# Optimization experiments

Measured on AMD Instinct MI355X. Metric: run time of the kernel, lower is better.

Reference implementation:

```python
import jax, jax.numpy as jnp
import numpy as np
from jax import lax

N_EXPERTS = 256
N_GROUP = 8
TOPK_GROUP = 4
TOP_K = 8
AUX_ALPHA = 0.001


def setup_inputs() -> dict:
    key = jax.random.key(0)
    k1, k2 = jax.random.split(key)
    hidden_states = jax.random.normal(k1, (16384, 2048), dtype=jnp.float32)
    weight = jax.random.normal(k2, (N_EXPERTS, 2048), dtype=jnp.float32) * 0.02
    return {"hidden_states": hidden_states, "weight": weight}


def reference(hidden_states, weight):
    n_tokens = hidden_states.shape[0]
    group_size = N_EXPERTS // N_GROUP  # 32

    # gating logits: [N, E]
    logits = jnp.einsum('nh,eh->ne', hidden_states, weight)

    # group-restricted top-k: [N, G, group_size] -> top TOPK_GROUP per group
    group_logits = logits.reshape(n_tokens, N_GROUP, group_size)
    gw, gi = lax.top_k(group_logits, TOPK_GROUP)          # [N, G, tg]
    gw = gw.reshape(n_tokens, N_GROUP * TOPK_GROUP)
    gi = gi.reshape(n_tokens, N_GROUP * TOPK_GROUP)

    # global top-k over the pooled group winners
    topk_weights, ti = lax.top_k(gw, TOP_K)               # [N, K]
    selected_group = ti // TOPK_GROUP
    expert_in_group = jnp.take_along_axis(gi, ti, axis=1)
    topk_idx = selected_group * group_size + expert_in_group  # [N, K]

    # norm_topk_prob=True
    topk_weights = topk_weights / (jnp.sum(topk_weights, axis=-1, keepdims=True) + 1e-20)

    # auxiliary load-balancing loss (training path)
    expert_mask = jax.nn.one_hot(topk_idx.reshape(-1), N_EXPERTS, dtype=jnp.float32)
    expert_counts = expert_mask.mean(axis=0)              # [E]
    expert_probs = jax.nn.softmax(logits, axis=-1).mean(axis=0)  # [E]
    aux_loss = jnp.sum(expert_counts * expert_probs) * AUX_ALPHA

    return topk_idx, topk_weights, aux_loss
```

## Files before the change

kernel.cpp:

```cpp
#include <hip/hip_runtime.h>
#include <math.h>

#define NTOK 16384
#define KD   2048
#define NE   256
#define BM   32
#define NSTEP 64
#define EPS  2.5e-4f

using bf16x8 = __attribute__((ext_vector_type(8))) short;
using f32x16 = __attribute__((ext_vector_type(16))) float;
using u16 = unsigned short;
using u32 = unsigned int;

__device__ __forceinline__ u16 f2bf(float x) {
    u32 u = __float_as_uint(x);
    return (u16)((u + 0x7FFFu + ((u >> 16) & 1u)) >> 16);
}
__device__ __forceinline__ float bf2f(u16 h) {
    return __uint_as_float(((u32)h) << 16);
}

__global__ __launch_bounds__(256) void wsplit_kernel(
    const float* __restrict__ wgt, u16* __restrict__ Whi, u16* __restrict__ Wlo)
{
    const int idx = blockIdx.x * 256 + threadIdx.x;
    const int e  = idx >> 8;
    const int ko = idx & 255;
    const int k  = ko * 8;
    const int c  = k >> 5, s = (k >> 4) & 1, kh = (k >> 3) & 1;
    const int dst = (c * 2 + s) * 4096 + (e >> 5) * 512 + kh * 256 + (e & 31) * 8;
    const float* p = wgt + (size_t)e * KD + k;
    u16 hi[8], lo[8];
#pragma unroll
    for (int i = 0; i < 8; ++i) {
        const float w = p[i];
        hi[i] = f2bf(w);
        lo[i] = f2bf(w - bf2f(hi[i]));
    }
    *(uint4*)(Whi + dst) = *(const uint4*)hi;
    *(uint4*)(Wlo + dst) = *(const uint4*)lo;
}

#define MFMA32(A, B, C) __builtin_amdgcn_mfma_f32_32x32x16_bf16((A), (B), (C), 0, 0, 0)

__global__ __launch_bounds__(256) void gate_kernel(
    const float* __restrict__ hid, const u16* __restrict__ Whi, const u16* __restrict__ Wlo,
    float* __restrict__ out, float* __restrict__ cnt, float* __restrict__ prb,
    int* __restrict__ flagcnt, int* __restrict__ flaglist)
{
    __shared__ float ls[BM][257];
    __shared__ float maxS[BM], sumS[BM], invS[BM];

    const int tid  = threadIdx.x;
    const int lane = tid & 63;
    const int wv   = tid >> 6;
    const int ln31 = lane & 31;
    const int kh   = lane >> 5;
    const int t0   = blockIdx.x * BM;

    f32x16 acc[2];
#pragma unroll
    for (int nf = 0; nf < 2; ++nf)
#pragma unroll
        for (int r = 0; r < 16; ++r) acc[nf][r] = 0.f;

    const float* arow = hid + (size_t)(t0 + ln31) * KD + kh * 8;
    const u16* bh_base = Whi + (wv * 2) * 512 + kh * 256 + ln31 * 8;
    const u16* bl_base = Wlo + (wv * 2) * 512 + kh * 256 + ln31 * 8;

#pragma unroll 2
    for (int c = 0; c < NSTEP; ++c) {
#pragma unroll
        for (int s = 0; s < 2; ++s) {
            const float* ap = arow + c * 32 + s * 16;
            const float4 a0 = *(const float4*)(ap);
            const float4 a1 = *(const float4*)(ap + 4);
            const float f[8] = {a0.x, a0.y, a0.z, a0.w, a1.x, a1.y, a1.z, a1.w};
            bf16x8 ah, al;
#pragma unroll
            for (int i = 0; i < 8; ++i) {
                const u16 h = f2bf(f[i]);
                ah[i] = (short)h;
                al[i] = (short)f2bf(f[i] - bf2f(h));
            }
            const int bo = (c * 2 + s) * 4096;
            const bf16x8 bh0 = *(const bf16x8*)(bh_base + bo);
            const bf16x8 bl0 = *(const bf16x8*)(bl_base + bo);
            const bf16x8 bh1 = *(const bf16x8*)(bh_base + bo + 512);
            const bf16x8 bl1 = *(const bf16x8*)(bl_base + bo + 512);
            acc[0] = MFMA32(ah, bh0, acc[0]);
            acc[0] = MFMA32(ah, bl0, acc[0]);
            acc[0] = MFMA32(al, bh0, acc[0]);
            acc[1] = MFMA32(ah, bh1, acc[1]);
            acc[1] = MFMA32(ah, bl1, acc[1]);
            acc[1] = MFMA32(al, bh1, acc[1]);
        }
    }

#pragma unroll
    for (int nf = 0; nf < 2; ++nf) {
        const int col = wv * 64 + nf * 32 + ln31;
#pragma unroll
        for (int r = 0; r < 16; ++r) {
            const int row = (r & 3) + 8 * (r >> 2) + 4 * (lane >> 5);
            ls[row][col] = acc[nf][r];
        }
    }
    if (tid < BM) sumS[tid] = 0.f;
    __syncthreads();

    if (tid < BM) {
        const float* lr = &ls[tid][0];
        float tv[9]; int ti[9];
#pragma unroll
        for (int j = 0; j < 9; ++j) { tv[j] = -1e30f; ti[j] = 0; }
        float gv3[8], gv4[8];
        float rowmax = -1e30f;

        auto ins9 = [&](float v, int idx) {
#pragma unroll
            for (int p = 0; p < 9; ++p) {
                if (v > tv[p]) {
#pragma unroll
                    for (int q = 8; q > p; --q) { tv[q] = tv[q - 1]; ti[q] = ti[q - 1]; }
                    tv[p] = v; ti[p] = idx;
                    break;
                }
            }
        };

#pragma unroll 1
        for (int g = 0; g < 8; ++g) {
            float v0 = -1e30f, v1 = -1e30f, v2 = -1e30f, v3 = -1e30f, v4 = -1e30f;
            int   i0 = 0, i1 = 0, i2 = 0, i3 = 0;
            for (int j = 0; j < 32; ++j) {
                const float v = lr[g * 32 + j];
                if (v > v0)      { v4=v3; v3=v2;i3=i2; v2=v1;i2=i1; v1=v0;i1=i0; v0=v;i0=j; }
                else if (v > v1) { v4=v3; v3=v2;i3=i2; v2=v1;i2=i1; v1=v;i1=j; }
                else if (v > v2) { v4=v3; v3=v2;i3=i2; v2=v;i2=j; }
                else if (v > v3) { v4=v3; v3=v;i3=j; }
                else if (v > v4) { v4=v; }
            }
            rowmax = fmaxf(rowmax, v0);
            gv3[g] = v3; gv4[g] = v4;
            ins9(v0, g * 32 + i0);
            ins9(v1, g * 32 + i1);
            ins9(v2, g * 32 + i2);
            ins9(v3, g * 32 + i3);
        }

        bool flag = false;
#pragma unroll
        for (int r = 0; r < 8; ++r)
            if (tv[r] - tv[r + 1] < EPS) flag = true;
#pragma unroll
        for (int g = 0; g < 8; ++g)
            if (gv3[g] - gv4[g] < EPS && gv3[g] > tv[7] - EPS) flag = true;

        const float s01 = __fadd_rn(tv[0], tv[1]);
        const float s23 = __fadd_rn(tv[2], tv[3]);
        const float s45 = __fadd_rn(tv[4], tv[5]);
        const float s67 = __fadd_rn(tv[6], tv[7]);
        float s = __fadd_rn(__fadd_rn(s01, s23), __fadd_rn(s45, s67));
        s = __fadd_rn(s, 1e-20f);

        const size_t tg2 = (size_t)(t0 + tid);
#pragma unroll
        for (int j = 0; j < 8; ++j) {
            out[tg2 * 8 + j]                    = (float)ti[j];
            out[(size_t)NTOK * 8 + tg2 * 8 + j] = __fdiv_rn(tv[j], s);
            atomicAdd(&cnt[ti[j]], 1.0f);
        }
        if (flag) {
            const int fi = atomicAdd(flagcnt, 1);
            flaglist[fi] = t0 + tid;
        }
        maxS[tid] = rowmax;
    }
    __syncthreads();

    {
        const int t  = tid >> 3;
        const int c0 = (tid & 7) * 32;
        const float m = maxS[t];
        float part = 0.f;
#pragma unroll
        for (int j = 0; j < 32; ++j) part += __expf(ls[t][c0 + j] - m);
        atomicAdd(&sumS[t], part);
    }
    __syncthreads();
    if (tid < BM) invS[tid] = 1.0f / sumS[tid];
    __syncthreads();

    {
        float p = 0.f;
#pragma unroll 4
        for (int n = 0; n < BM; ++n) p += __expf(ls[n][tid] - maxS[n]) * invS[n];
        atomicAdd(&prb[tid], p);
    }
}

__global__ __launch_bounds__(1024) void exact_kernel(
    const float* __restrict__ hid, const float* __restrict__ wgt,
    float* __restrict__ out, float* __restrict__ cnt,
    const int* __restrict__ flagcnt, const int* __restrict__ flaglist)
{
    const int fn = *flagcnt;

    __shared__ float wch[256 * 17];
    __shared__ float hch[32 * 17];
    __shared__ float exls[32][257];
    __shared__ int tk[32];

    const int tid = threadIdx.x;
    const int tg  = tid >> 7;
    const int eg  = (tid >> 2) & 31;
    const int l   = tid & 3;

#pragma unroll 1
    for (int base = blockIdx.x * 32; base < fn; base += gridDim.x * 32) {
        const int nt = min(32, fn - base);
        __syncthreads();
        if (tid < 32) tk[tid] = (tid < nt) ? flaglist[base + tid] : flaglist[base];
        __syncthreads();

        float accq[4][8];
#pragma unroll
        for (int i = 0; i < 4; ++i)
#pragma unroll
            for (int j = 0; j < 8; ++j) accq[i][j] = 0.f;

#pragma unroll 1
        for (int c = 0; c < 128; ++c) {
            __syncthreads();
            {
                const int e  = tid >> 2;
                const int q4 = (tid & 3) * 4;
                const float4 w = *(const float4*)(wgt + (size_t)e * KD + c * 16 + q4);
                float* wr = &wch[e * 17 + q4];
                wr[0] = w.x; wr[1] = w.y; wr[2] = w.z; wr[3] = w.w;
            }
            if (tid < 512) {
                const int tok = tid >> 4, k = tid & 15;
                hch[tok * 17 + k] = hid[(size_t)tk[tok] * KD + c * 16 + k];
            }
            __syncthreads();

#pragma unroll
            for (int q = 3; q >= 0; --q) {
                const int k = 4 * q + l;
                float hv[4], wv2[8];
#pragma unroll
                for (int i = 0; i < 4; ++i) hv[i] = hch[(tg * 4 + i) * 17 + k];
#pragma unroll
                for (int j = 0; j < 8; ++j) wv2[j] = wch[(j * 32 + eg) * 17 + k];
#pragma unroll
                for (int i = 0; i < 4; ++i)
#pragma unroll
                    for (int j = 0; j < 8; ++j)
                        accq[i][j] = __fadd_rn(__fmul_rn(hv[i], wv2[j]), accq[i][j]);
            }
        }

        __syncthreads();
#pragma unroll
        for (int i = 0; i < 4; ++i)
#pragma unroll
            for (int j = 0; j < 8; ++j) {
                float v = accq[i][j];
                v = __fadd_rn(v, __shfl_xor(v, 1));
                v = __fadd_rn(v, __shfl_xor(v, 2));
                if (l == 0) exls[tg * 4 + i][j * 32 + eg] = v;
            }
        __syncthreads();

        if (tid < nt) {
            const float* lr = &exls[tid][0];
            float tv[8]; int ti[8];
#pragma unroll
            for (int j = 0; j < 8; ++j) { tv[j] = -1e30f; ti[j] = 0; }

            auto ins8 = [&](float v, int idx) {
#pragma unroll
                for (int p = 0; p < 8; ++p) {
                    if (v > tv[p]) {
#pragma unroll
                        for (int q = 7; q > p; --q) { tv[q] = tv[q - 1]; ti[q] = ti[q - 1]; }
                        tv[p] = v; ti[p] = idx;
                        break;
                    }
                }
            };

#pragma unroll 1
            for (int g = 0; g < 8; ++g) {
                float v0 = -1e30f, v1 = -1e30f, v2 = -1e30f, v3 = -1e30f;
                int   i0 = 0, i1 = 0, i2 = 0, i3 = 0;
                for (int j = 0; j < 32; ++j) {
                    const float v = lr[g * 32 + j];
                    if (v > v0)      { v3=v2;i3=i2; v2=v1;i2=i1; v1=v0;i1=i0; v0=v;i0=j; }
                    else if (v > v1) { v3=v2;i3=i2; v2=v1;i2=i1; v1=v;i1=j; }
                    else if (v > v2) { v3=v2;i3=i2; v2=v;i2=j; }
                    else if (v > v3) { v3=v;i3=j; }
                }
                ins8(v0, g * 32 + i0);
                ins8(v1, g * 32 + i1);
                ins8(v2, g * 32 + i2);
                ins8(v3, g * 32 + i3);
            }

            const float s01 = __fadd_rn(tv[0], tv[1]);
            const float s23 = __fadd_rn(tv[2], tv[3]);
            const float s45 = __fadd_rn(tv[4], tv[5]);
            const float s67 = __fadd_rn(tv[6], tv[7]);
            float s = __fadd_rn(__fadd_rn(s01, s23), __fadd_rn(s45, s67));
            s = __fadd_rn(s, 1e-20f);

            const size_t gt = (size_t)tk[tid];
#pragma unroll
            for (int j = 0; j < 8; ++j) {
                const int oldi = (int)out[gt * 8 + j];
                if (oldi != ti[j]) {
                    atomicAdd(&cnt[oldi], -1.0f);
                    atomicAdd(&cnt[ti[j]], 1.0f);
                }
                out[gt * 8 + j]                    = (float)ti[j];
                out[(size_t)NTOK * 8 + gt * 8 + j] = __fdiv_rn(tv[j], s);
            }
        }
        __syncthreads();
    }
}

__global__ void aux_kernel(const float* __restrict__ cnt,
                           const float* __restrict__ prb,
                           float* __restrict__ out)
{
    const int tid = threadIdx.x;
    float v = cnt[tid] * prb[tid];
#pragma unroll
    for (int off = 32; off; off >>= 1) v += __shfl_down(v, off, 64);
    __shared__ float ps[4];
    if ((tid & 63) == 0) ps[tid >> 6] = v;
    __syncthreads();
    if (tid == 0) {
        const float tot = ps[0] + ps[1] + ps[2] + ps[3];
        out[(size_t)NTOK * 8 * 2] = tot * (0.001f / (131072.0f * 16384.0f));
    }
}

extern "C" void kernel_launch(void* const* d_in, const int* in_sizes, int n_in,
                              void* d_out, int out_size, void* d_ws, size_t ws_size,
                              hipStream_t stream)
{
    (void)in_sizes; (void)n_in; (void)out_size; (void)ws_size;
    const float* hid = (const float*)d_in[0];
    const float* wgt = (const float*)d_in[1];
    float* out = (float*)d_out;

    float* cnt      = (float*)d_ws;
    float* prb      = cnt + NE;
    int*   flagcnt  = (int*)(prb + NE);
    int*   flaglist = flagcnt + 64;
    u16*   Whi      = (u16*)(flaglist + NTOK);
    u16*   Wlo      = Whi + (size_t)NE * KD;

    hipMemsetAsync(d_ws, 0, (2 * NE + 64) * sizeof(float), stream);
    wsplit_kernel<<<NE * KD / 8 / 256, 256, 0, stream>>>(wgt, Whi, Wlo);
    gate_kernel<<<NTOK / BM, 256, 0, stream>>>(hid, Whi, Wlo, out, cnt, prb, flagcnt, flaglist);
    exact_kernel<<<128, 1024, 0, stream>>>(hid, wgt, out, cnt, flagcnt, flaglist);
    aux_kernel<<<1, 256, 0, stream>>>(cnt, prb, out);
}
```

Before: 593.0 us.

## Split gate GEMM K across four wave groups; shrink exact-kernel token batches

The gate kernel now runs 1024 threads per block, with four groups of waves each covering a quarter of the K dimension. Their partial accumulators are summed into shared memory in turns separated by barriers, and the softmax stages are remapped to the larger thread count. The exact recompute kernel moves to 256-thread blocks handling 8 flagged tokens each on a grid of 2048, which spreads the few flagged tokens over more CUs. The cost is extra shared-memory reduction passes and barriers in the gate kernel, plus more redundant weight-chunk loads per token in the exact kernel.

```diff
diff --git a/kernel.cpp b/kernel.cpp
--- a/kernel.cpp
+++ b/kernel.cpp
@@ -44,7 +44,7 @@
 
 #define MFMA32(A, B, C) __builtin_amdgcn_mfma_f32_32x32x16_bf16((A), (B), (C), 0, 0, 0)
 
-__global__ __launch_bounds__(256) void gate_kernel(
+__global__ __launch_bounds__(1024) void gate_kernel(
     const float* __restrict__ hid, const u16* __restrict__ Whi, const u16* __restrict__ Wlo,
     float* __restrict__ out, float* __restrict__ cnt, float* __restrict__ prb,
     int* __restrict__ flagcnt, int* __restrict__ flaglist)
@@ -55,6 +55,8 @@
     const int tid  = threadIdx.x;
     const int lane = tid & 63;
     const int wv   = tid >> 6;
+    const int cs   = wv & 3;
+    const int kq   = wv >> 2;
     const int ln31 = lane & 31;
     const int kh   = lane >> 5;
     const int t0   = blockIdx.x * BM;
@@ -66,11 +68,13 @@
         for (int r = 0; r < 16; ++r) acc[nf][r] = 0.f;
 
     const float* arow = hid + (size_t)(t0 + ln31) * KD + kh * 8;
-    const u16* bh_base = Whi + (wv * 2) * 512 + kh * 256 + ln31 * 8;
-    const u16* bl_base = Wlo + (wv * 2) * 512 + kh * 256 + ln31 * 8;
-
+    const u16* bh_base = Whi + (cs * 2) * 512 + kh * 256 + ln31 * 8;
+    const u16* bl_base = Wlo + (cs * 2) * 512 + kh * 256 + ln31 * 8;
+
+    const int cbeg = kq * (NSTEP / 4);
+    const int cend = cbeg + NSTEP / 4;
 #pragma unroll 2
-    for (int c = 0; c < NSTEP; ++c) {
+    for (int c = cbeg; c < cend; ++c) {
 #pragma unroll
         for (int s = 0; s < 2; ++s) {
             const float* ap = arow + c * 32 + s * 16;
@@ -98,14 +102,32 @@
         }
     }
 
-#pragma unroll
-    for (int nf = 0; nf < 2; ++nf) {
-        const int col = wv * 64 + nf * 32 + ln31;
-#pragma unroll
-        for (int r = 0; r < 16; ++r) {
-            const int row = (r & 3) + 8 * (r >> 2) + 4 * (lane >> 5);
-            ls[row][col] = acc[nf][r];
-        }
+    if (kq == 0) {
+#pragma unroll
+        for (int nf = 0; nf < 2; ++nf) {
+            const int col = cs * 64 + nf * 32 + ln31;
+#pragma unroll
+            for (int r = 0; r < 16; ++r) {
+                const int row = (r & 3) + 8 * (r >> 2) + 4 * kh;
+                ls[row][col] = acc[nf][r];
+            }
+        }
+    }
+    __syncthreads();
+#pragma unroll 1
+    for (int q = 1; q < 4; ++q) {
+        if (kq == q) {
+#pragma unroll
+            for (int nf = 0; nf < 2; ++nf) {
+                const int col = cs * 64 + nf * 32 + ln31;
+#pragma unroll
+                for (int r = 0; r < 16; ++r) {
+                    const int row = (r & 3) + 8 * (r >> 2) + 4 * kh;
+                    ls[row][col] += acc[nf][r];
+                }
+            }
+        }
+        __syncthreads();
     }
     if (tid < BM) sumS[tid] = 0.f;
     __syncthreads();
@@ -181,19 +203,19 @@
     __syncthreads();
 
     {
-        const int t  = tid >> 3;
-        const int c0 = (tid & 7) * 32;
+        const int t  = tid >> 5;
+        const int c0 = (tid & 31) * 8;
         const float m = maxS[t];
         float part = 0.f;
 #pragma unroll
-        for (int j = 0; j < 32; ++j) part += __expf(ls[t][c0 + j] - m);
+        for (int j = 0; j < 8; ++j) part += __expf(ls[t][c0 + j] - m);
         atomicAdd(&sumS[t], part);
     }
     __syncthreads();
     if (tid < BM) invS[tid] = 1.0f / sumS[tid];
     __syncthreads();
 
-    {
+    if (tid < NE) {
         float p = 0.f;
 #pragma unroll 4
         for (int n = 0; n < BM; ++n) p += __expf(ls[n][tid] - maxS[n]) * invS[n];
@@ -201,7 +223,7 @@
     }
 }
 
-__global__ __launch_bounds__(1024) void exact_kernel(
+__global__ __launch_bounds__(256) void exact_kernel(
     const float* __restrict__ hid, const float* __restrict__ wgt,
     float* __restrict__ out, float* __restrict__ cnt,
     const int* __restrict__ flagcnt, const int* __restrict__ flaglist)
@@ -209,9 +231,9 @@
     const int fn = *flagcnt;
 
     __shared__ float wch[256 * 17];
-    __shared__ float hch[32 * 17];
-    __shared__ float exls[32][257];
-    __shared__ int tk[32];
+    __shared__ float hch[8 * 17];
+    __shared__ float exls[8][257];
+    __shared__ int tk[8];
 
     const int tid = threadIdx.x;
     const int tg  = tid >> 7;
@@ -219,10 +241,10 @@
     const int l   = tid & 3;
 
 #pragma unroll 1
-    for (int base = blockIdx.x * 32; base < fn; base += gridDim.x * 32) {
-        const int nt = min(32, fn - base);
-        __syncthreads();
-        if (tid < 32) tk[tid] = (tid < nt) ? flaglist[base + tid] : flaglist[base];
+    for (int base = blockIdx.x * 8; base < fn; base += gridDim.x * 8) {
+        const int nt = min(8, fn - base);
+        __syncthreads();
+        if (tid < 8) tk[tid] = (tid < nt) ? flaglist[base + tid] : flaglist[base];
         __syncthreads();
 
         float accq[4][8];
@@ -235,13 +257,18 @@
         for (int c = 0; c < 128; ++c) {
             __syncthreads();
             {
-                const int e  = tid >> 2;
-                const int q4 = (tid & 3) * 4;
-                const float4 w = *(const float4*)(wgt + (size_t)e * KD + c * 16 + q4);
-                float* wr = &wch[e * 17 + q4];
-                wr[0] = w.x; wr[1] = w.y; wr[2] = w.z; wr[3] = w.w;
-            }
-            if (tid < 512) {
+                const float* p = wgt + (size_t)tid * KD + c * 16;
+                float4 w0 = *(const float4*)(p);
+                float4 w1 = *(const float4*)(p + 4);
+                float4 w2 = *(const float4*)(p + 8);
+                float4 w3 = *(const float4*)(p + 12);
+                float* wr = &wch[tid * 17];
+                wr[0]=w0.x; wr[1]=w0.y; wr[2]=w0.z; wr[3]=w0.w;
+                wr[4]=w1.x; wr[5]=w1.y; wr[6]=w1.z; wr[7]=w1.w;
+                wr[8]=w2.x; wr[9]=w2.y; wr[10]=w2.z; wr[11]=w2.w;
+                wr[12]=w3.x; wr[13]=w3.y; wr[14]=w3.z; wr[15]=w3.w;
+            }
+            if (tid < 128) {
                 const int tok = tid >> 4, k = tid & 15;
                 hch[tok * 17 + k] = hid[(size_t)tk[tok] * KD + c * 16 + k];
             }
@@ -368,7 +395,7 @@
 
     hipMemsetAsync(d_ws, 0, (2 * NE + 64) * sizeof(float), stream);
     wsplit_kernel<<<NE * KD / 8 / 256, 256, 0, stream>>>(wgt, Whi, Wlo);
-    gate_kernel<<<NTOK / BM, 256, 0, stream>>>(hid, Whi, Wlo, out, cnt, prb, flagcnt, flaglist);
-    exact_kernel<<<128, 1024, 0, stream>>>(hid, wgt, out, cnt, flagcnt, flaglist);
+    gate_kernel<<<NTOK / BM, 1024, 0, stream>>>(hid, Whi, Wlo, out, cnt, prb, flagcnt, flaglist);
+    exact_kernel<<<2048, 256, 0, stream>>>(hid, wgt, out, cnt, flagcnt, flaglist);
     aux_kernel<<<1, 256, 0, stream>>>(cnt, prb, out);
 }
```

Measured after the change: 576.3 us. 1.03x faster.
